# Optimization experiments

Measured on AMD Instinct MI355X. Metric: run time of the kernel, lower is better.

Reference implementation:

```python
import jax, jax.numpy as jnp
import numpy as np


def setup_inputs() -> dict:
    key = jax.random.key(0)
    ks = jax.random.split(key, 7)
    Bsz, Dm, L, N = 2, 1536, 2048, 16
    x = jax.random.normal(ks[0], (Bsz, Dm, L), jnp.float32)
    delta = jax.random.uniform(ks[1], (Bsz, Dm, L), jnp.float32, 1e-3, 0.1)  # positive step sizes
    A = -jax.random.uniform(ks[2], (Dm, N), jnp.float32, 0.5, 1.5)  # negative real A for stability
    B = jax.random.normal(ks[3], (Bsz, N, L), jnp.float32)
    C = jax.random.normal(ks[4], (Bsz, N, L), jnp.float32)
    D = jax.random.normal(ks[5], (Dm,), jnp.float32)
    z = jax.random.normal(ks[6], (Bsz, Dm, L), jnp.float32)
    return {"x": x, "delta": delta, "A": A, "B": B, "C": C, "D": D, "z": z}


def reference(x, delta, A, B, C, D, z):
    # x, delta, z: [b, d, l]; A: [d, n]; B, C: [b, n, l]; D: [d]
    dtype_in = x.dtype
    x = x.astype(jnp.float32)
    delta = delta.astype(jnp.float32)
    Bm = B.astype(jnp.float32)
    Cm = C.astype(jnp.float32)

    # time-major for scan: [l, b, ...]
    dl = jnp.moveaxis(delta, 2, 0)   # l b d
    xl = jnp.moveaxis(x, 2, 0)       # l b d
    Bl = jnp.moveaxis(Bm, 2, 0)      # l b n
    Cl = jnp.moveaxis(Cm, 2, 0)      # l b n

    h0 = jnp.zeros((x.shape[0], A.shape[0], A.shape[1]), jnp.float32)  # b d n

    def step(h, inp):
        d_t, x_t, B_t, C_t = inp
        deltaA = jnp.exp(d_t[:, :, None] * A[None, :, :])      # exp(einsum('bdl,dn->bdln')) at token t
        deltaB = d_t[:, :, None] * B_t[:, None, :]              # einsum('bdl,bnl->bdln') at token t
        h = deltaA * h + deltaB * x_t[:, :, None]               # Hx update
        y = jnp.einsum('bdn,bn->bd', h, C_t)                    # Yh readout
        return h, y

    _, ys = jax.lax.scan(step, h0, (dl, xl, Bl, Cl))            # ys: [l, b, d]
    y = jnp.moveaxis(ys, 0, 2)                                  # b d l

    out = y + x * D[None, :, None]
    out = out * jax.nn.silu(z)
    return out.astype(dtype_in)
```

## Files before the change

### kernel.cpp

```cpp
#include <hip/hip_runtime.h>
#include <hip/hip_fp16.h>

#define LOG2E 1.44269504088896340736f
#define DM 1536
#define LL  2048
#define NN  16
#define NCH 128
#define CL  16

__device__ __forceinline__ float fexp2(float v){ return __builtin_amdgcn_exp2f(v); }
__device__ __forceinline__ float frcp(float v){ return __builtin_amdgcn_rcpf(v); }

__device__ __forceinline__ float packdx(float d, float x){
    unsigned u = (unsigned)__half_as_ushort(__float2half_rn(d))
               | ((unsigned)__half_as_ushort(__float2half_rn(x)) << 16);
    return __uint_as_float(u);
}
__device__ __forceinline__ void unpackdx(float f, float& d, float& x){
    const unsigned u = __float_as_uint(f);
    d = __half2float(__ushort_as_half((unsigned short)(u & 0xffffu)));
    x = __half2float(__ushort_as_half((unsigned short)(u >> 16)));
}
__device__ __forceinline__ void unpack8(const float4 f, float* o){
    const unsigned u0=__float_as_uint(f.x), u1=__float_as_uint(f.y),
                   u2=__float_as_uint(f.z), u3=__float_as_uint(f.w);
    o[0]=__half2float(__ushort_as_half((unsigned short)(u0&0xffffu)));
    o[1]=__half2float(__ushort_as_half((unsigned short)(u0>>16)));
    o[2]=__half2float(__ushort_as_half((unsigned short)(u1&0xffffu)));
    o[3]=__half2float(__ushort_as_half((unsigned short)(u1>>16)));
    o[4]=__half2float(__ushort_as_half((unsigned short)(u2&0xffffu)));
    o[5]=__half2float(__ushort_as_half((unsigned short)(u2>>16)));
    o[6]=__half2float(__ushort_as_half((unsigned short)(u3&0xffffu)));
    o[7]=__half2float(__ushort_as_half((unsigned short)(u3>>16)));
}

__global__ __launch_bounds__(256) void transpose_bc(
        const float* __restrict__ Bm, const float* __restrict__ Cm,
        __half* __restrict__ BC){
    const int q  = blockIdx.x*256 + threadIdx.x;
    const int t0 = (q & 511) << 2;
    const int n  = (q >> 9) & 15;
    const int b  = q >> 13;
    const long i = (long)(b*NN + n)*LL + t0;
    const float4 bv = *(const float4*)(Bm + i);
    const float4 cv = *(const float4*)(Cm + i);
    const float bb[4]={bv.x,bv.y,bv.z,bv.w}, cc[4]={cv.x,cv.y,cv.z,cv.w};
#pragma unroll
    for (int j=0;j<4;++j){
        const int t = t0 + j;
        const long o = ((long)((b*CL + (t&15))*NCH + (t>>4)))*32 + n;
        BC[o]      = __float2half_rn(bb[j]);
        BC[o + 16] = __float2half_rn(cc[j]);
    }
}

__global__ __launch_bounds__(128, 3) void ssm_scan(
    const float* __restrict__ x, const float* __restrict__ delta,
    const float* __restrict__ A, const float* __restrict__ Dv,
    const float* __restrict__ z, const __half* __restrict__ BC,
    float* __restrict__ out)
{
    __shared__ float2 sdx[CL*NCH];
    __shared__ float  wtot[2][2][NN];

    const int lane = threadIdx.x & 63;
    const int w    = threadIdx.x >> 6;
    const int row0 = blockIdx.x*2;
    const int b    = (row0 >= DM) ? 1 : 0;
    const int d0   = row0 - b*DM;
    const int cmy  = w*64 + lane;

    const long base0 = (long)row0*LL;
    const long base1 = base0 + LL;
    const float* gd0 = delta + base0; const float* gx0 = x + base0;
    const float* gd1 = delta + base1; const float* gx1 = x + base1;

    for (int k=0;k<1024;k+=256){
        const int t0 = w*1024 + k + lane*4;
        const float4 dv0 = *(const float4*)(gd0 + t0);
        const float4 xv0 = *(const float4*)(gx0 + t0);
        const float4 dv1 = *(const float4*)(gd1 + t0);
        const float4 xv1 = *(const float4*)(gx1 + t0);
        const float dd0[4]={dv0.x,dv0.y,dv0.z,dv0.w}, xx0[4]={xv0.x,xv0.y,xv0.z,xv0.w};
        const float dd1[4]={dv1.x,dv1.y,dv1.z,dv1.w}, xx1[4]={xv1.x,xv1.y,xv1.z,xv1.w};
#pragma unroll
        for (int j=0;j<4;++j){
            const int t = t0 + j, r = t & 15, c = t >> 4;
            float2 wd; wd.x = packdx(dd0[j], xx0[j]); wd.y = packdx(dd1[j], xx1[j]);
            sdx[r*NCH + (c^r)] = wd;
        }
    }

    float A20[NN], A21[NN];
#pragma unroll
    for (int n=0;n<NN;++n){
        A20[n] = A[d0*NN+n]     * LOG2E;
        A21[n] = A[(d0+1)*NN+n] * LOG2E;
    }

    const __half* bc = BC + (long)b*65536 + cmy*32;

    float G0[NN], G1[NN];
#pragma unroll
    for (int n=0;n<NN;++n){ G0[n]=0.f; G1[n]=0.f; }
    float ds0=0.f, ds1=0.f;
#pragma unroll 2
    for (int r=0;r<CL;++r){
        const float2 wd = sdx[r*NCH + (cmy^r)];
        const float4* rec = (const float4*)(bc + (long)r*4096);
        float bb[16];
        unpack8(rec[0], bb); unpack8(rec[1], bb+8);
        float d_0,x_0,d_1,x_1;
        unpackdx(wd.x, d_0, x_0); unpackdx(wd.y, d_1, x_1);
        ds0 += d_0; ds1 += d_1;
        const float dx0 = d_0*x_0, dx1 = d_1*x_1;
#pragma unroll
        for (int n=0;n<NN;++n){
            const float e0 = fexp2(d_0*A20[n]);
            G0[n] = __builtin_fmaf(e0, G0[n], bb[n]*dx0);
            const float e1 = fexp2(d_1*A21[n]);
            G1[n] = __builtin_fmaf(e1, G1[n], bb[n]*dx1);
        }
    }

    float h0[NN], h1[NN];
    {
        float P0[NN], P1[NN];
#pragma unroll
        for (int n=0;n<NN;++n){ P0[n]=fexp2(ds0*A20[n]); P1[n]=fexp2(ds1*A21[n]); }
#pragma unroll
        for (int s=1;s<64;s<<=1){
#pragma unroll
            for (int n=0;n<NN;++n){
                const float pl0=__shfl_up(P0[n],s), gl0=__shfl_up(G0[n],s);
                const float pl1=__shfl_up(P1[n],s), gl1=__shfl_up(G1[n],s);
                if (lane >= s){
                    G0[n]=__builtin_fmaf(P0[n],gl0,G0[n]); P0[n]*=pl0;
                    G1[n]=__builtin_fmaf(P1[n],gl1,G1[n]); P1[n]*=pl1;
                }
            }
        }
        if (w==0 && lane==63){
#pragma unroll
            for (int n=0;n<NN;++n){
                wtot[0][0][n]=P0[n]; wtot[1][0][n]=G0[n];
                wtot[0][1][n]=P1[n]; wtot[1][1][n]=G1[n];
            }
        }
        __syncthreads();
#pragma unroll
        for (int n=0;n<NN;++n){
            const float pe0=__shfl_up(P0[n],1), ge0=__shfl_up(G0[n],1);
            const float pe1=__shfl_up(P1[n],1), ge1=__shfl_up(G1[n],1);
            const float Px0 = (lane==0)?1.f:pe0, Gx0 = (lane==0)?0.f:ge0;
            const float Px1 = (lane==0)?1.f:pe1, Gx1 = (lane==0)?0.f:ge1;
            const float Gt0 = (w==0)?0.f:wtot[1][0][n];
            const float Gt1 = (w==0)?0.f:wtot[1][1][n];
            h0[n] = __builtin_fmaf(Px0, Gt0, Gx0);
            h1[n] = __builtin_fmaf(Px1, Gt1, Gx1);
        }
    }

    const float Dd0 = Dv[d0], Dd1 = Dv[d0+1];
#pragma unroll 2
    for (int r=0;r<CL;++r){
        const int slot = r*NCH + (cmy^r);
        const float2 wd = sdx[slot];
        const float4* rec = (const float4*)(bc + (long)r*4096);
        float bb[16], cc[16];
        unpack8(rec[0], bb); unpack8(rec[1], bb+8);
        unpack8(rec[2], cc); unpack8(rec[3], cc+8);
        float d_0,x_0,d_1,x_1;
        unpackdx(wd.x, d_0, x_0); unpackdx(wd.y, d_1, x_1);
        const float dx0 = d_0*x_0, dx1 = d_1*x_1;
        float ya0=0.f, yb0=0.f, ya1=0.f, yb1=0.f;
#pragma unroll
        for (int n=0;n<NN;n+=2){
            const float e0a = fexp2(d_0*A20[n]);
            h0[n]  =__builtin_fmaf(e0a,h0[n],  bb[n]*dx0);   ya0=__builtin_fmaf(h0[n],  cc[n],  ya0);
            const float e0b = fexp2(d_0*A20[n+1]);
            h0[n+1]=__builtin_fmaf(e0b,h0[n+1],bb[n+1]*dx0); yb0=__builtin_fmaf(h0[n+1],cc[n+1],yb0);
            const float e1a = fexp2(d_1*A21[n]);
            h1[n]  =__builtin_fmaf(e1a,h1[n],  bb[n]*dx1);   ya1=__builtin_fmaf(h1[n],  cc[n],  ya1);
            const float e1b = fexp2(d_1*A21[n+1]);
            h1[n+1]=__builtin_fmaf(e1b,h1[n+1],bb[n+1]*dx1); yb1=__builtin_fmaf(h1[n+1],cc[n+1],yb1);
        }
        float2 yo;
        yo.x = __builtin_fmaf(x_0, Dd0, ya0+yb0);
        yo.y = __builtin_fmaf(x_1, Dd1, ya1+yb1);
        sdx[slot] = yo;
    }

    const float* gz0 = z + base0; const float* gz1 = z + base1;
    float* go0 = out + base0;     float* go1 = out + base1;
    for (int k=0;k<1024;k+=256){
        const int t0 = w*1024 + k + lane*4;
        const float4 zv0 = *(const float4*)(gz0 + t0);
        const float4 zv1 = *(const float4*)(gz1 + t0);
        const float zz0[4]={zv0.x,zv0.y,zv0.z,zv0.w}, zz1[4]={zv1.x,zv1.y,zv1.z,zv1.w};
        float o0[4], o1[4];
#pragma unroll
        for (int j=0;j<4;++j){
            const int t = t0 + j, r = t & 15, c = t >> 4;
            const float2 wd = sdx[r*NCH + (c^r)];
            const float s0 = frcp(1.f + fexp2(-zz0[j]*LOG2E));
            const float s1 = frcp(1.f + fexp2(-zz1[j]*LOG2E));
            o0[j] = wd.x * (zz0[j]*s0);
            o1[j] = wd.y * (zz1[j]*s1);
        }
        float4 a  = {o0[0],o0[1],o0[2],o0[3]};
        float4 bq = {o1[0],o1[1],o1[2],o1[3]};
        *(float4*)(go0 + t0) = a;
        *(float4*)(go1 + t0) = bq;
    }
}

extern "C" void kernel_launch(void* const* d_in, const int* in_sizes, int n_in,
                              void* d_out, int out_size, void* d_ws, size_t ws_size,
                              hipStream_t stream) {
    const float* x     = (const float*)d_in[0];
    const float* delta = (const float*)d_in[1];
    const float* A     = (const float*)d_in[2];
    const float* B     = (const float*)d_in[3];
    const float* C     = (const float*)d_in[4];
    const float* Dv    = (const float*)d_in[5];
    const float* z     = (const float*)d_in[6];
    float* out = (float*)d_out;

    __half* BC = (__half*)d_ws;

    transpose_bc<<<dim3(64), dim3(256), 0, stream>>>(B, C, BC);
    ssm_scan<<<dim3(DM), dim3(128), 0, stream>>>(x, delta, A, Dv, z, BC, out);
}
```

Baseline: 155.4 us.

## Split scan into 256 chunks of 8 across four waves per block

Doubles the number of sequence chunks per row pair from 128 to 256, so each block runs four waves over chunks of 8 timesteps. The cross-wave carry now combines per-wave totals from shared memory with a short serial loop. The XOR swizzle on the shared staging buffer is dropped, and the half-pack/unpack helpers now use half2 intrinsics. The aim is more parallelism and shorter serial chains per thread, paid for with more cross-chunk combine work and possible LDS bank conflicts.

New measurement: 275.7 us. 1.77x slower.

```diff
diff --git a/kernel.cpp b/kernel.cpp
--- a/kernel.cpp
+++ b/kernel.cpp
@@ -5,33 +5,25 @@
 #define DM 1536
 #define LL  2048
 #define NN  16
-#define NCH 128
-#define CL  16
+#define NCH 256
+#define CL  8
 
 __device__ __forceinline__ float fexp2(float v){ return __builtin_amdgcn_exp2f(v); }
 __device__ __forceinline__ float frcp(float v){ return __builtin_amdgcn_rcpf(v); }
 
 __device__ __forceinline__ float packdx(float d, float x){
-    unsigned u = (unsigned)__half_as_ushort(__float2half_rn(d))
-               | ((unsigned)__half_as_ushort(__float2half_rn(x)) << 16);
-    return __uint_as_float(u);
+    return __builtin_bit_cast(float, __floats2half2_rn(d, x));
 }
 __device__ __forceinline__ void unpackdx(float f, float& d, float& x){
-    const unsigned u = __float_as_uint(f);
-    d = __half2float(__ushort_as_half((unsigned short)(u & 0xffffu)));
-    x = __half2float(__ushort_as_half((unsigned short)(u >> 16)));
+    const float2 p = __half22float2(__builtin_bit_cast(__half2, f));
+    d = p.x; x = p.y;
 }
 __device__ __forceinline__ void unpack8(const float4 f, float* o){
-    const unsigned u0=__float_as_uint(f.x), u1=__float_as_uint(f.y),
-                   u2=__float_as_uint(f.z), u3=__float_as_uint(f.w);
-    o[0]=__half2float(__ushort_as_half((unsigned short)(u0&0xffffu)));
-    o[1]=__half2float(__ushort_as_half((unsigned short)(u0>>16)));
-    o[2]=__half2float(__ushort_as_half((unsigned short)(u1&0xffffu)));
-    o[3]=__half2float(__ushort_as_half((unsigned short)(u1>>16)));
-    o[4]=__half2float(__ushort_as_half((unsigned short)(u2&0xffffu)));
-    o[5]=__half2float(__ushort_as_half((unsigned short)(u2>>16)));
-    o[6]=__half2float(__ushort_as_half((unsigned short)(u3&0xffffu)));
-    o[7]=__half2float(__ushort_as_half((unsigned short)(u3>>16)));
+    float2 p;
+    p = __half22float2(__builtin_bit_cast(__half2, f.x)); o[0]=p.x; o[1]=p.y;
+    p = __half22float2(__builtin_bit_cast(__half2, f.y)); o[2]=p.x; o[3]=p.y;
+    p = __half22float2(__builtin_bit_cast(__half2, f.z)); o[4]=p.x; o[5]=p.y;
+    p = __half22float2(__builtin_bit_cast(__half2, f.w)); o[6]=p.x; o[7]=p.y;
 }
 
 __global__ __launch_bounds__(256) void transpose_bc(
@@ -48,35 +40,36 @@
 #pragma unroll
     for (int j=0;j<4;++j){
         const int t = t0 + j;
-        const long o = ((long)((b*CL + (t&15))*NCH + (t>>4)))*32 + n;
+        const long o = ((long)((b*CL + (t&7))*NCH + (t>>3)))*32 + n;
         BC[o]      = __float2half_rn(bb[j]);
         BC[o + 16] = __float2half_rn(cc[j]);
     }
 }
 
-__global__ __launch_bounds__(128, 3) void ssm_scan(
+__global__ __launch_bounds__(256, 6) void ssm_scan(
     const float* __restrict__ x, const float* __restrict__ delta,
     const float* __restrict__ A, const float* __restrict__ Dv,
     const float* __restrict__ z, const __half* __restrict__ BC,
     float* __restrict__ out)
 {
     __shared__ float2 sdx[CL*NCH];
-    __shared__ float  wtot[2][2][NN];
+    __shared__ float  wtP[4][2][NN];
+    __shared__ float  wtG[4][2][NN];
 
     const int lane = threadIdx.x & 63;
     const int w    = threadIdx.x >> 6;
+    const int cmy  = threadIdx.x;
     const int row0 = blockIdx.x*2;
     const int b    = (row0 >= DM) ? 1 : 0;
     const int d0   = row0 - b*DM;
-    const int cmy  = w*64 + lane;
 
     const long base0 = (long)row0*LL;
     const long base1 = base0 + LL;
     const float* gd0 = delta + base0; const float* gx0 = x + base0;
     const float* gd1 = delta + base1; const float* gx1 = x + base1;
 
-    for (int k=0;k<1024;k+=256){
-        const int t0 = w*1024 + k + lane*4;
+    for (int k=0;k<512;k+=256){
+        const int t0 = w*512 + k + lane*4;
         const float4 dv0 = *(const float4*)(gd0 + t0);
         const float4 xv0 = *(const float4*)(gx0 + t0);
         const float4 dv1 = *(const float4*)(gd1 + t0);
@@ -85,9 +78,9 @@
         const float dd1[4]={dv1.x,dv1.y,dv1.z,dv1.w}, xx1[4]={xv1.x,xv1.y,xv1.z,xv1.w};
 #pragma unroll
         for (int j=0;j<4;++j){
-            const int t = t0 + j, r = t & 15, c = t >> 4;
+            const int t = t0 + j, r = t & 7, c = t >> 3;
             float2 wd; wd.x = packdx(dd0[j], xx0[j]); wd.y = packdx(dd1[j], xx1[j]);
-            sdx[r*NCH + (c^r)] = wd;
+            sdx[r*NCH + c] = wd;
         }
     }
 
@@ -106,8 +99,8 @@
     float ds0=0.f, ds1=0.f;
 #pragma unroll 2
     for (int r=0;r<CL;++r){
-        const float2 wd = sdx[r*NCH + (cmy^r)];
-        const float4* rec = (const float4*)(bc + (long)r*4096);
+        const float2 wd = sdx[r*NCH + cmy];
+        const float4* rec = (const float4*)(bc + (long)r*8192);
         float bb[16];
         unpack8(rec[0], bb); unpack8(rec[1], bb+8);
         float d_0,x_0,d_1,x_1;
@@ -140,11 +133,11 @@
                 }
             }
         }
-        if (w==0 && lane==63){
+        if (lane==63){
 #pragma unroll
             for (int n=0;n<NN;++n){
-                wtot[0][0][n]=P0[n]; wtot[1][0][n]=G0[n];
-                wtot[0][1][n]=P1[n]; wtot[1][1][n]=G1[n];
+                wtP[w][0][n]=P0[n]; wtG[w][0][n]=G0[n];
+                wtP[w][1][n]=P1[n]; wtG[w][1][n]=G1[n];
             }
         }
         __syncthreads();
@@ -154,19 +147,22 @@
             const float pe1=__shfl_up(P1[n],1), ge1=__shfl_up(G1[n],1);
             const float Px0 = (lane==0)?1.f:pe0, Gx0 = (lane==0)?0.f:ge0;
             const float Px1 = (lane==0)?1.f:pe1, Gx1 = (lane==0)?0.f:ge1;
-            const float Gt0 = (w==0)?0.f:wtot[1][0][n];
-            const float Gt1 = (w==0)?0.f:wtot[1][1][n];
-            h0[n] = __builtin_fmaf(Px0, Gt0, Gx0);
-            h1[n] = __builtin_fmaf(Px1, Gt1, Gx1);
+            float gp0 = 0.f, gp1 = 0.f;
+            for (int wv=0; wv<w; ++wv){
+                gp0 = __builtin_fmaf(wtP[wv][0][n], gp0, wtG[wv][0][n]);
+                gp1 = __builtin_fmaf(wtP[wv][1][n], gp1, wtG[wv][1][n]);
+            }
+            h0[n] = __builtin_fmaf(Px0, gp0, Gx0);
+            h1[n] = __builtin_fmaf(Px1, gp1, Gx1);
         }
     }
 
     const float Dd0 = Dv[d0], Dd1 = Dv[d0+1];
 #pragma unroll 2
     for (int r=0;r<CL;++r){
-        const int slot = r*NCH + (cmy^r);
+        const int slot = r*NCH + cmy;
         const float2 wd = sdx[slot];
-        const float4* rec = (const float4*)(bc + (long)r*4096);
+        const float4* rec = (const float4*)(bc + (long)r*8192);
         float bb[16], cc[16];
         unpack8(rec[0], bb); unpack8(rec[1], bb+8);
         unpack8(rec[2], cc); unpack8(rec[3], cc+8);
@@ -193,16 +189,16 @@
 
     const float* gz0 = z + base0; const float* gz1 = z + base1;
     float* go0 = out + base0;     float* go1 = out + base1;
-    for (int k=0;k<1024;k+=256){
-        const int t0 = w*1024 + k + lane*4;
+    for (int k=0;k<512;k+=256){
+        const int t0 = w*512 + k + lane*4;
         const float4 zv0 = *(const float4*)(gz0 + t0);
         const float4 zv1 = *(const float4*)(gz1 + t0);
         const float zz0[4]={zv0.x,zv0.y,zv0.z,zv0.w}, zz1[4]={zv1.x,zv1.y,zv1.z,zv1.w};
         float o0[4], o1[4];
 #pragma unroll
         for (int j=0;j<4;++j){
-            const int t = t0 + j, r = t & 15, c = t >> 4;
-            const float2 wd = sdx[r*NCH + (c^r)];
+            const int t = t0 + j, r = t & 7, c = t >> 3;
+            const float2 wd = sdx[r*NCH + c];
             const float s0 = frcp(1.f + fexp2(-zz0[j]*LOG2E));
             const float s1 = frcp(1.f + fexp2(-zz1[j]*LOG2E));
             o0[j] = wd.x * (zz0[j]*s0);
@@ -230,5 +226,5 @@
     __half* BC = (__half*)d_ws;
 
     transpose_bc<<<dim3(64), dim3(256), 0, stream>>>(B, C, BC);
-    ssm_scan<<<dim3(DM), dim3(128), 0, stream>>>(x, delta, A, Dv, z, BC, out);
-}
+    ssm_scan<<<dim3(DM), dim3(256), 0, stream>>>(x, delta, A, Dv, z, BC, out);
+}
```
